# Optimization experiments

Measured on AMD Instinct MI355X. Metric: run time of the kernel, lower is better.

## Reference

```python
import jax, jax.numpy as jnp
import numpy as np

# dims (see shape_source): emb_dim=256, input_size=256 -> d_model=1024
B, L = 8, 1024
QUES = 4000
EMB = 256
DM = 1024          # input_size + 768
DI = 2048          # expand * d_model
N = 16             # d_state
DTR = 64           # dt_rank = ceil(d_model/16)
K = 4              # d_conv
EPS = 1e-12


def setup_inputs() -> dict:
    key = jax.random.key(0)
    ks = jax.random.split(key, 16)
    s = 0.02
    nrm = lambda k, sh: jax.random.normal(k, sh, dtype=jnp.float32) * s
    return {
        "x": jax.random.randint(ks[0], (B, L), 0, 2 * QUES + 1),
        "q_id": jax.random.randint(ks[1], (B, L), 0, QUES),
        "emb_table": nrm(ks[2], (2 * QUES + 1, EMB)),
        "ques_cont": nrm(ks[3], (QUES, 768)),
        "ln0_g": jnp.ones((DM,), jnp.float32),
        "ln0_b": jnp.zeros((DM,), jnp.float32),
        "in_proj_w": nrm(ks[4], (2 * DI, DM)),
        "conv_w": nrm(ks[5], (DI, K)),
        "conv_b": jnp.zeros((DI,), jnp.float32),
        "x_proj_w": nrm(ks[6], (DTR + 2 * N, DI)),
        "dt_proj_w": nrm(ks[7], (DI, DTR)),
        "dt_proj_b": nrm(ks[8], (DI,)),
        "A_log": jnp.log(jax.random.uniform(ks[9], (DI, N), jnp.float32, 1.0, 16.0)),
        "D_param": jnp.ones((DI,), jnp.float32),
        "out_proj_w": nrm(ks[10], (DM, DI)),
        "ln1_g": jnp.ones((DM,), jnp.float32),
        "ln1_b": jnp.zeros((DM,), jnp.float32),
        "fc_w": nrm(ks[11], (QUES, DM)),
        "fc_b": jnp.zeros((QUES,), jnp.float32),
    }


def _ln(x, g, b):
    m = x.mean(-1, keepdims=True)
    v = ((x - m) ** 2).mean(-1, keepdims=True)
    return (x - m) / jnp.sqrt(v + EPS) * g + b


def _mamba(xm, in_proj_w, conv_w, conv_b, x_proj_w, dt_proj_w, dt_proj_b,
           A_log, D_param, out_proj_w):
    # xm: [B, L, DM]
    u_r = xm @ in_proj_w.T                           # [B, L, 2*DI]
    u, r = jnp.split(u_r, 2, axis=-1)                # each [B, L, DI]
    Lq = u.shape[1]
    # causal depthwise conv1d (padding=K-1, truncated to L)
    u_pad = jnp.pad(u, ((0, 0), (K - 1, 0), (0, 0)))
    conv = sum(u_pad[:, k:k + Lq, :] * conv_w[:, k] for k in range(K)) + conv_b
    u = jax.nn.silu(conv)
    dbl = u @ x_proj_w.T                             # [B, L, DTR+2N]
    dt, Bm, Cm = dbl[..., :DTR], dbl[..., DTR:DTR + N], dbl[..., DTR + N:]
    delta = jax.nn.softplus(dt @ dt_proj_w.T + dt_proj_b)   # [B, L, DI]
    A = -jnp.exp(A_log)                              # [DI, N]

    def step(h, ins):
        d_t, b_t, c_t, u_t = ins                     # [B,DI],[B,N],[B,N],[B,DI]
        dA = jnp.exp(d_t[:, :, None] * A)            # [B, DI, N]
        h = dA * h + d_t[:, :, None] * b_t[:, None, :] * u_t[:, :, None]
        y_t = jnp.einsum('bdn,bn->bd', h, c_t)
        return h, y_t

    xs = (delta.transpose(1, 0, 2), Bm.transpose(1, 0, 2),
          Cm.transpose(1, 0, 2), u.transpose(1, 0, 2))
    h0 = jnp.zeros((u.shape[0], DI, N), u.dtype)
    _, ys = jax.lax.scan(step, h0, xs)               # ys: [L, B, DI]
    y = ys.transpose(1, 0, 2) + u * D_param
    y = y * jax.nn.silu(r)
    return y @ out_proj_w.T                          # [B, L, DM]


def reference(x, q_id, emb_table, ques_cont, ln0_g, ln0_b, in_proj_w, conv_w,
              conv_b, x_proj_w, dt_proj_w, dt_proj_b, A_log, D_param,
              out_proj_w, ln1_g, ln1_b, fc_w, fc_b):
    x_e = emb_table[x]                               # [B, L, 256]
    x_c = ques_cont[q_id]                            # [B, L, 768]
    item = _ln(jnp.concatenate([x_e, x_c], axis=-1), ln0_g, ln0_b)
    # source loop applies every layer to item_emb; only the last layer's
    # output is used, so compute exactly that one layer (num_layers=2 branch).
    h = _mamba(item, in_proj_w, conv_w, conv_b, x_proj_w, dt_proj_w,
               dt_proj_b, A_log, D_param, out_proj_w)
    out = _ln(h + item, ln1_g, ln1_b)
    return jax.nn.sigmoid(out @ fc_w.T + fc_b)       # [B, L, QUES]
```

## Files before the change

### kernel.cpp

```cpp
#include <hip/hip_runtime.h>
#include <cstdint>
#include <cstddef>

#define L_SEQ 1024
#define BATCH 8
#define DMODEL 1024
#define DINNER 2048
#define NSTATE 16
#define DTRANK 64
#define NQ 4000
#define NROWS (BATCH * L_SEQ)
#define CH 32
#define NCH (L_SEQ / CH)

typedef float f32x4 __attribute__((ext_vector_type(4)));
typedef __bf16 bf16x8 __attribute__((ext_vector_type(8)));

#define AS1 __attribute__((address_space(1)))
#define AS3 __attribute__((address_space(3)))

#define VMCNT(n) asm volatile("s_waitcnt vmcnt(" #n ")" ::: "memory")
#define SBARRIER() asm volatile("s_barrier" ::: "memory")

__device__ __forceinline__ unsigned short f2bf(float f) {
  union { float f; unsigned int u; } c; c.f = f;
  unsigned int u = c.u;
  unsigned int r = u + 0x7fffu + ((u >> 16) & 1u);
  return (unsigned short)(r >> 16);
}

__device__ __forceinline__ float sigmoidf_(float x) { return 1.f / (1.f + expf(-x)); }

__global__ void cast_bf16_k(const float* __restrict__ src, unsigned short* __restrict__ dst, int n) {
  int i = blockIdx.x * blockDim.x + threadIdx.x;
  if (i < n) dst[i] = f2bf(src[i]);
}

__device__ __forceinline__ float blk_sum(float v, float* s) {
  #pragma unroll
  for (int o = 32; o > 0; o >>= 1) v += __shfl_down(v, o, 64);
  int w = threadIdx.x >> 6;
  if ((threadIdx.x & 63) == 0) s[w] = v;
  __syncthreads();
  float r = s[0] + s[1] + s[2] + s[3];
  __syncthreads();
  return r;
}

__global__ __launch_bounds__(256) void embed_ln0_k(
    const int* __restrict__ x, const int* __restrict__ qid,
    const float* __restrict__ emb, const float* __restrict__ qc,
    const float* __restrict__ g, const float* __restrict__ bta,
    float* __restrict__ item, unsigned short* __restrict__ item_bf)
{
  __shared__ float sbuf[4];
  int i = blockIdx.x;
  int t = threadIdx.x;
  float4 v;
  if (t < 64) v = *(const float4*)&emb[(size_t)x[i] * 256 + t * 4];
  else        v = *(const float4*)&qc[(size_t)qid[i] * 768 + t * 4 - 256];
  float tot = blk_sum(v.x + v.y + v.z + v.w, sbuf);
  float mean = tot * (1.f / 1024.f);
  float dx = v.x - mean, dy = v.y - mean, dz = v.z - mean, dw = v.w - mean;
  float var = blk_sum(dx*dx + dy*dy + dz*dz + dw*dw, sbuf) * (1.f / 1024.f);
  float rstd = rsqrtf(var + 1e-12f);
  float vals[4] = {dx, dy, dz, dw};
  size_t rb = (size_t)i * 1024;
  #pragma unroll
  for (int j = 0; j < 4; j++) {
    int c = t * 4 + j;
    float o = vals[j] * rstd * g[c] + bta[c];
    item[rb + c] = o;
    item_bf[rb + c] = f2bf(o);
  }
}

template <int EPI>
__global__ __launch_bounds__(256) void gemm_bt_k(
    const unsigned short* __restrict__ A, const unsigned short* __restrict__ Bw,
    float* __restrict__ C, const float* __restrict__ bias,
    unsigned short* __restrict__ aux,
    int M, int N, int K)
{
  __shared__ __align__(16) unsigned short As[128 * 64];
  __shared__ __align__(16) unsigned short Bs[128 * 64];
  const int tid = threadIdx.x;
  const int m0 = blockIdx.x * 128;
  const int n0 = blockIdx.y * 128;
  const int w = tid >> 6, lane = tid & 63;
  const int wrow = (w >> 1) * 64, wcol = (w & 1) * 64;
  const int quad = lane >> 4, lid = lane & 15;

  const int srow = lane >> 3;
  const int schunk = (lane & 7) ^ srow;

  const unsigned short* Abase = A + (size_t)(m0 + w * 8 + srow) * K + schunk * 8;
  const unsigned short* Bbase[4];
  #pragma unroll
  for (int i = 0; i < 4; i++) {
    int rB = n0 + w * 8 + i * 32 + srow;
    if (rB > N - 1) rB = N - 1;
    Bbase[i] = Bw + (size_t)rB * K + schunk * 8;
  }

  f32x4 acc[4][4] = {};

  for (int k0 = 0; k0 < K; k0 += 64) {
    #pragma unroll
    for (int i = 0; i < 4; i++) {
      int rA = w * 8 + i * 32;
      __builtin_amdgcn_global_load_lds(
          (const AS1 unsigned int*)(Abase + (size_t)i * 32 * K + k0),
          (AS3 unsigned int*)&As[rA * 64], 16, 0, 0);
      __builtin_amdgcn_global_load_lds(
          (const AS1 unsigned int*)(Bbase[i] + k0),
          (AS3 unsigned int*)&Bs[rA * 64], 16, 0, 0);
    }
    __syncthreads();
    #pragma unroll
    for (int kk = 0; kk < 64; kk += 32) {
      bf16x8 af[4], bfr[4];
      #pragma unroll
      for (int mi = 0; mi < 4; mi++) {
        int r = wrow + mi * 16 + lid;
        int slot = ((kk >> 3) + quad) ^ (lid & 7);
        af[mi] = *(const bf16x8*)&As[r * 64 + slot * 8];
      }
      #pragma unroll
      for (int ni = 0; ni < 4; ni++) {
        int r = wcol + ni * 16 + lid;
        int slot = ((kk >> 3) + quad) ^ (lid & 7);
        bfr[ni] = *(const bf16x8*)&Bs[r * 64 + slot * 8];
      }
      #pragma unroll
      for (int mi = 0; mi < 4; mi++)
        #pragma unroll
        for (int ni = 0; ni < 4; ni++)
          acc[mi][ni] = __builtin_amdgcn_mfma_f32_16x16x32_bf16(af[mi], bfr[ni], acc[mi][ni], 0, 0, 0);
    }
    __syncthreads();
  }

  #pragma unroll
  for (int mi = 0; mi < 4; mi++) {
    #pragma unroll
    for (int ni = 0; ni < 4; ni++) {
      int col = n0 + wcol + ni * 16 + lid;
      if (col >= N) continue;
      #pragma unroll
      for (int r = 0; r < 4; r++) {
        int row = m0 + wrow + mi * 16 + quad * 4 + r;
        float v = acc[mi][ni][r];
        if (EPI == 1) v = sigmoidf_(v + bias[col]);
        if (EPI == 2) { float xx = v + bias[col]; v = fmaxf(xx, 0.f) + log1pf(expf(-fabsf(xx))); }
        C[(size_t)row * N + col] = v;
        if (EPI == 3 && col < 64) aux[(size_t)row * 64 + col] = f2bf(v);
      }
    }
  }
}

template <int BN, int EPI>
__global__ __launch_bounds__(512, 2) void gemm_pipe_k(
    const unsigned short* __restrict__ A, const unsigned short* __restrict__ Bw,
    float* __restrict__ C, const float* __restrict__ bias,
    int M, int N, int K)
{
  constexpr int NB = BN / 64;
  constexpr int BJ = (BN == 256) ? 2 : 1;
  constexpr int NI = 2 + BJ;

  __shared__ __align__(16) unsigned short As[3][256 * 32];
  __shared__ __align__(16) unsigned short Bs[3][BN * 32];

  const int tid = threadIdx.x;
  const int gx = gridDim.x;
  const int nwg = gx * gridDim.y;
  int bid = blockIdx.y * gx + blockIdx.x;
  bid = (bid & 7) * (nwg >> 3) + (bid >> 3);
  const int m0 = (bid % gx) * 256;
  const int n0 = (bid / gx) * BN;

  const int w = tid >> 6, lane = tid & 63;
  const int wm = w >> 2, wn = w & 3;
  const int quad = lane >> 4, lid = lane & 15;

  const int srow = lane >> 2;
  const int sch  = ((lane & 3) ^ ((lane >> 3) & 3)) * 8;

  const unsigned short* Ag[2];
  int AsegE[2];
  #pragma unroll
  for (int j = 0; j < 2; j++) {
    Ag[j] = A + (size_t)(m0 + 32 * w + 16 * j + srow) * K + sch;
    AsegE[j] = (w * 2 + j) * 512;
  }
  const unsigned short* Bg[BJ];
  int BsegE[BJ];
  #pragma unroll
  for (int j = 0; j < BJ; j++) {
    int rB = n0 + (BN == 256 ? 32 * w + 16 * j : 16 * w) + srow;
    if (rB > N - 1) rB = N - 1;
    Bg[j] = Bw + (size_t)rB * K + sch;
    BsegE[j] = (BN == 256 ? (w * 2 + j) : w) * 512;
  }

  auto stage = [&](int buf, int t) {
    const int ko = t * 32;
    #pragma unroll
    for (int j = 0; j < 2; j++)
      __builtin_amdgcn_global_load_lds(
          (const AS1 unsigned int*)(Ag[j] + ko),
          (AS3 unsigned int*)&As[buf][AsegE[j]], 16, 0, 0);
    #pragma unroll
    for (int j = 0; j < BJ; j++)
      __builtin_amdgcn_global_load_lds(
          (const AS1 unsigned int*)(Bg[j] + ko),
          (AS3 unsigned int*)&Bs[buf][BsegE[j]], 16, 0, 0);
  };

  const int slot8 = (quad ^ ((lid >> 1) & 3)) * 8;
  const int aoff = (wm * 128 + lid) * 32 + slot8;
  const int boff = (wn * (BN / 4) + lid) * 32 + slot8;

  f32x4 acc[8][NB] = {};
  const int nt = K >> 5;

  stage(0, 0);
  stage(1, 1);
  if constexpr (NI == 4) VMCNT(4); else VMCNT(3);
  SBARRIER();

  int bR = 0, bS = 2;
  for (int t = 0; t < nt; ++t) {
    const bool more = (t + 2 < nt);
    if (more) stage(bS, t + 2);
    __builtin_amdgcn_sched_barrier(0);

    bf16x8 af[8], bfr[NB];
    #pragma unroll
    for (int ni = 0; ni < NB; ni++) bfr[ni] = *(const bf16x8*)&Bs[bR][boff + ni * 512];
    #pragma unroll
    for (int mi = 0; mi < 8; mi++)  af[mi]  = *(const bf16x8*)&As[bR][aoff + mi * 512];

    __builtin_amdgcn_s_setprio(1);
    #pragma unroll
    for (int mi = 0; mi < 8; mi++)
      #pragma unroll
      for (int ni = 0; ni < NB; ni++)
        acc[mi][ni] = __builtin_amdgcn_mfma_f32_16x16x32_bf16(af[mi], bfr[ni], acc[mi][ni], 0, 0, 0);
    __builtin_amdgcn_s_setprio(0);

    __builtin_amdgcn_sched_barrier(0);
    if (more) { if constexpr (NI == 4) VMCNT(4); else VMCNT(3); }
    else VMCNT(0);
    SBARRIER();
    bR = (bR + 1 == 3) ? 0 : bR + 1;
    bS = (bS + 1 == 3) ? 0 : bS + 1;
  }

  #pragma unroll
  for (int mi = 0; mi < 8; mi++) {
    #pragma unroll
    for (int ni = 0; ni < NB; ni++) {
      int col = n0 + wn * (BN / 4) + ni * 16 + lid;
      if (col >= N) continue;
      #pragma unroll
      for (int r = 0; r < 4; r++) {
        int row = m0 + wm * 128 + mi * 16 + quad * 4 + r;
        float v = acc[mi][ni][r];
        if (EPI == 1) v = sigmoidf_(v + bias[col]);
        C[(size_t)row * N + col] = v;
      }
    }
  }
}

__global__ void conv_silu_k(const float* __restrict__ u_r, const float* __restrict__ w,
                            const float* __restrict__ cb, float* __restrict__ uc,
                            unsigned short* __restrict__ uc_bf)
{
  int idx = blockIdx.x * blockDim.x + threadIdx.x;
  if (idx >= BATCH * L_SEQ * DINNER) return;
  int d = idx & (DINNER - 1);
  int l = (idx >> 11) & (L_SEQ - 1);
  int b = idx >> 21;
  float4 wv = ((const float4*)w)[d];
  size_t rb = ((size_t)b * L_SEQ + l) * (2 * DINNER) + d;
  float acc = cb[d];
  acc += wv.w * u_r[rb];
  if (l >= 1) acc += wv.z * u_r[rb - (2 * DINNER)];
  if (l >= 2) acc += wv.y * u_r[rb - 2 * (2 * DINNER)];
  if (l >= 3) acc += wv.x * u_r[rb - 3 * (2 * DINNER)];
  float s = acc * sigmoidf_(acc);
  uc[idx] = s;
  uc_bf[idx] = f2bf(s);
}

__global__ void a2_k(const float* __restrict__ Alog, float* __restrict__ a2t)
{
  int i = blockIdx.x * blockDim.x + threadIdx.x;
  if (i >= DINNER * NSTATE) return;
  int d = i >> 4, n = i & 15;
  a2t[n * DINNER + d] = -expf(Alog[i]) * 1.4426950408889634f;
}

__global__ __launch_bounds__(64) void scan1_k(
    const float* __restrict__ dlt, const float* __restrict__ uc,
    const float* __restrict__ dbl, const float* __restrict__ a2t,
    float* __restrict__ Pbuf, float* __restrict__ Qbuf)
{
  int c = blockIdx.x;
  int dg = blockIdx.y;
  int b = blockIdx.z;
  int d = dg * 64 + threadIdx.x;
  float a2[NSTATE], P[NSTATE], q[NSTATE];
  #pragma unroll
  for (int n = 0; n < NSTATE; n++) {
    a2[n] = a2t[n * DINNER + d];
    P[n] = 1.f; q[n] = 0.f;
  }
  size_t base = ((size_t)(b * L_SEQ + c * CH)) * DINNER + d;
  const float* bc = dbl + (size_t)(b * L_SEQ + c * CH) * 96 + 64;
  for (int t = 0; t < CH; t++) {
    float dl = dlt[base];
    float du = dl * uc[base];
    #pragma unroll
    for (int n = 0; n < NSTATE; n++) {
      float dA = exp2f(dl * a2[n]);
      q[n] = dA * q[n] + du * bc[n];
      P[n] *= dA;
    }
    base += DINNER;
    bc += 96;
  }
  size_t ob = ((size_t)((b * NCH + c) * NSTATE)) * DINNER + d;
  #pragma unroll
  for (int n = 0; n < NSTATE; n++) {
    Pbuf[ob + (size_t)n * DINNER] = P[n];
    Qbuf[ob + (size_t)n * DINNER] = q[n];
  }
}

__global__ void scan_carry_k(const float* __restrict__ Pbuf, float* __restrict__ Qbuf)
{
  int idx = blockIdx.x * blockDim.x + threadIdx.x;
  if (idx >= BATCH * NSTATE * DINNER) return;
  int d = idx & (DINNER - 1);
  int n = (idx >> 11) & 15;
  int b = idx >> 15;
  float h = 0.f;
  for (int c = 0; c < NCH; c++) {
    size_t o = ((size_t)((b * NCH + c) * NSTATE + n)) * DINNER + d;
    float P = Pbuf[o];
    float q = Qbuf[o];
    Qbuf[o] = h;
    h = P * h + q;
  }
}

__global__ __launch_bounds__(64) void scan2_k(
    const float* __restrict__ dlt, const float* __restrict__ uc,
    const float* __restrict__ dbl, const float* __restrict__ a2t,
    const float* __restrict__ Qbuf, const float* __restrict__ u_r,
    const float* __restrict__ Dp, unsigned short* __restrict__ ybf)
{
  int c = blockIdx.x;
  int dg = blockIdx.y;
  int b = blockIdx.z;
  int d = dg * 64 + threadIdx.x;
  float a2[NSTATE], h[NSTATE];
  size_t ob = ((size_t)((b * NCH + c) * NSTATE)) * DINNER + d;
  #pragma unroll
  for (int n = 0; n < NSTATE; n++) {
    a2[n] = a2t[n * DINNER + d];
    h[n] = Qbuf[ob + (size_t)n * DINNER];
  }
  float Dd = Dp[d];
  size_t base = ((size_t)(b * L_SEQ + c * CH)) * DINNER + d;
  const float* bc = dbl + (size_t)(b * L_SEQ + c * CH) * 96 + 64;
  const float* rp = u_r + (size_t)(b * L_SEQ + c * CH) * (2 * DINNER) + DINNER + d;
  for (int t = 0; t < CH; t++) {
    float dl = dlt[base];
    float uval = uc[base];
    float du = dl * uval;
    float yv = 0.f;
    #pragma unroll
    for (int n = 0; n < NSTATE; n++) {
      float dA = exp2f(dl * a2[n]);
      h[n] = dA * h[n] + du * bc[n];
      yv += h[n] * bc[NSTATE + n];
    }
    float rv = *rp;
    float val = (yv + uval * Dd) * (rv * sigmoidf_(rv));
    ybf[base] = f2bf(val);
    base += DINNER;
    bc += 96;
    rp += 2 * DINNER;
  }
}

__global__ __launch_bounds__(256) void ln1_k(
    const float* __restrict__ mamba, const float* __restrict__ item,
    const float* __restrict__ g, const float* __restrict__ bta,
    unsigned short* __restrict__ out_bf)
{
  __shared__ float sbuf[4];
  int i = blockIdx.x;
  int t = threadIdx.x;
  size_t rb = (size_t)i * 1024 + t * 4;
  float4 v = *(const float4*)&mamba[rb];
  float4 w4 = *(const float4*)&item[rb];
  v.x += w4.x; v.y += w4.y; v.z += w4.z; v.w += w4.w;
  float tot = blk_sum(v.x + v.y + v.z + v.w, sbuf);
  float mean = tot * (1.f / 1024.f);
  float dx = v.x - mean, dy = v.y - mean, dz = v.z - mean, dw = v.w - mean;
  float var = blk_sum(dx*dx + dy*dy + dz*dz + dw*dw, sbuf) * (1.f / 1024.f);
  float rstd = rsqrtf(var + 1e-12f);
  float vals[4] = {dx, dy, dz, dw};
  #pragma unroll
  for (int j = 0; j < 4; j++) {
    int c = t * 4 + j;
    out_bf[(size_t)i * 1024 + c] = f2bf(vals[j] * rstd * g[c] + bta[c]);
  }
}

extern "C" void kernel_launch(void* const* d_in, const int* in_sizes, int n_in,
                              void* d_out, int out_size, void* d_ws, size_t ws_size,
                              hipStream_t stream)
{
  (void)in_sizes; (void)n_in; (void)out_size; (void)ws_size;
  const int*   x     = (const int*)d_in[0];
  const int*   qid   = (const int*)d_in[1];
  const float* emb   = (const float*)d_in[2];
  const float* qc    = (const float*)d_in[3];
  const float* ln0g  = (const float*)d_in[4];
  const float* ln0b  = (const float*)d_in[5];
  const float* w_in  = (const float*)d_in[6];
  const float* convw = (const float*)d_in[7];
  const float* convb = (const float*)d_in[8];
  const float* w_x   = (const float*)d_in[9];
  const float* w_dt  = (const float*)d_in[10];
  const float* dtb   = (const float*)d_in[11];
  const float* Alog  = (const float*)d_in[12];
  const float* Dp    = (const float*)d_in[13];
  const float* w_out = (const float*)d_in[14];
  const float* ln1g  = (const float*)d_in[15];
  const float* ln1b  = (const float*)d_in[16];
  const float* w_fc  = (const float*)d_in[17];
  const float* fcb   = (const float*)d_in[18];
  float* out = (float*)d_out;

  char* base = (char*)d_ws;
  size_t off = 0;
  auto carve = [&](size_t bytes) -> char* {
    char* p = base + off;
    off = (off + bytes + 255) & ~(size_t)255;
    return p;
  };
  float* item  = (float*)carve((size_t)NROWS * 1024 * 4);
  float* u_r   = (float*)carve((size_t)NROWS * 4096 * 4);
  float* uc    = (float*)carve((size_t)NROWS * 2048 * 4);
  float* dbl   = (float*)carve((size_t)NROWS * 96 * 4);
  float* dlt   = (float*)carve((size_t)NROWS * 2048 * 4);
  float* mamba = (float*)carve((size_t)NROWS * 1024 * 4);
  unsigned short* bfbuf  = (unsigned short*)carve((size_t)NROWS * 2048 * 2);
  unsigned short* bw_in  = (unsigned short*)carve((size_t)4096 * 1024 * 2);
  unsigned short* bw_x   = (unsigned short*)carve((size_t)96 * 2048 * 2);
  unsigned short* bw_dt  = (unsigned short*)carve((size_t)2048 * 64 * 2);
  unsigned short* bw_out = (unsigned short*)carve((size_t)1024 * 2048 * 2);
  unsigned short* bw_fc  = (unsigned short*)carve((size_t)4000 * 1024 * 2);
  float* a2t   = (float*)carve((size_t)DINNER * NSTATE * 4);

  unsigned short* dt_bf = (unsigned short*)mamba;
  float* Pbuf = mamba;
  float* Qbuf = (float*)bfbuf;
  unsigned short* y_bf = (unsigned short*)mamba;
  float* mamba_out = u_r;

  auto cv = [&](const float* s, unsigned short* dst, int n) {
    cast_bf16_k<<<(n + 255) / 256, 256, 0, stream>>>(s, dst, n);
  };
  cv(w_in,  bw_in,  4096 * 1024);
  cv(w_x,   bw_x,   96 * 2048);
  cv(w_dt,  bw_dt,  2048 * 64);
  cv(w_out, bw_out, 1024 * 2048);
  cv(w_fc,  bw_fc,  4000 * 1024);
  a2_k<<<(DINNER * NSTATE + 255) / 256, 256, 0, stream>>>(Alog, a2t);

  embed_ln0_k<<<NROWS, 256, 0, stream>>>(x, qid, emb, qc, ln0g, ln0b, item, bfbuf);

  gemm_pipe_k<256, 0><<<dim3(32, 16), 512, 0, stream>>>(bfbuf, bw_in, u_r, nullptr, NROWS, 4096, 1024);

  conv_silu_k<<<(NROWS * DINNER) / 256, 256, 0, stream>>>(u_r, convw, convb, uc, bfbuf);

  gemm_bt_k<3><<<dim3(64, 1), 256, 0, stream>>>(bfbuf, bw_x, dbl, nullptr, dt_bf, NROWS, 96, 2048);

  gemm_bt_k<2><<<dim3(64, 16), 256, 0, stream>>>(dt_bf, bw_dt, dlt, dtb, nullptr, NROWS, 2048, 64);

  scan1_k<<<dim3(NCH, 32, BATCH), 64, 0, stream>>>(dlt, uc, dbl, a2t, Pbuf, Qbuf);
  scan_carry_k<<<(BATCH * NSTATE * DINNER) / 256, 256, 0, stream>>>(Pbuf, Qbuf);
  scan2_k<<<dim3(NCH, 32, BATCH), 64, 0, stream>>>(dlt, uc, dbl, a2t, Qbuf, u_r, Dp, y_bf);

  gemm_pipe_k<128, 0><<<dim3(32, 8), 512, 0, stream>>>(y_bf, bw_out, mamba_out, nullptr, NROWS, 1024, 2048);

  ln1_k<<<NROWS, 256, 0, stream>>>(mamba_out, item, ln1g, ln1b, bfbuf);

  gemm_pipe_k<256, 1><<<dim3(32, 16), 512, 0, stream>>>(bfbuf, bw_fc, out, fcb, NROWS, 4000, 1024);
}
```

Baseline: 923.9 us.

## Restructure bf16 GEMM pipeline into 4-slice, 8-phase staging with split MFMA groups

Replaces the 3-buffer, one-K-tile-per-iteration GEMM loop with a 4-slice LDS layout that covers two K=32 tiles per iteration. The iteration is split into four phases. Each phase issues a separate A or B load unit and runs half of the MFMA block, with barriers between phases. The goal is finer interleaving of global-to-LDS loads with MFMA work and deeper prefetch, to hide memory latency in the three large GEMMs. The cost is more barriers per K step and more LDS per block, which could reduce occupancy.

Result: slower. 1.094 ms (+18.4%).

```diff
diff --git a/kernel.cpp b/kernel.cpp
--- a/kernel.cpp
+++ b/kernel.cpp
@@ -20,6 +20,7 @@
 #define AS3 __attribute__((address_space(3)))
 
 #define VMCNT(n) asm volatile("s_waitcnt vmcnt(" #n ")" ::: "memory")
+#define LGKMCNT0() asm volatile("s_waitcnt lgkmcnt(0)" ::: "memory")
 #define SBARRIER() asm volatile("s_barrier" ::: "memory")
 
 __device__ __forceinline__ unsigned short f2bf(float f) {
@@ -161,17 +162,18 @@
 }
 
 template <int BN, int EPI>
-__global__ __launch_bounds__(512, 2) void gemm_pipe_k(
+__global__ __launch_bounds__(512, 2) void gemm8p_k(
     const unsigned short* __restrict__ A, const unsigned short* __restrict__ Bw,
     float* __restrict__ C, const float* __restrict__ bias,
     int M, int N, int K)
 {
   constexpr int NB = BN / 64;
-  constexpr int BJ = (BN == 256) ? 2 : 1;
-  constexpr int NI = 2 + BJ;
-
-  __shared__ __align__(16) unsigned short As[3][256 * 32];
-  __shared__ __align__(16) unsigned short Bs[3][BN * 32];
+  constexpr int BJ = BN / 128;
+  constexpr int ASLICE = 256 * 32;
+  constexpr int BSLICE = BN * 32;
+
+  __shared__ __align__(16) unsigned short As[4 * ASLICE];
+  __shared__ __align__(16) unsigned short Bs[4 * BSLICE];
 
   const int tid = threadIdx.x;
   const int gx = gridDim.x;
@@ -185,38 +187,43 @@
   const int wm = w >> 2, wn = w & 3;
   const int quad = lane >> 4, lid = lane & 15;
 
-  const int srow = lane >> 2;
-  const int sch  = ((lane & 3) ^ ((lane >> 3) & 3)) * 8;
-
+  const int g8 = ((lane & 3) ^ ((lane >> 3) & 3)) * 8;
   const unsigned short* Ag[2];
   int AsegE[2];
   #pragma unroll
   for (int j = 0; j < 2; j++) {
-    Ag[j] = A + (size_t)(m0 + 32 * w + 16 * j + srow) * K + sch;
+    Ag[j] = A + (size_t)(m0 + w * 32 + j * 16 + (lane >> 2)) * K + g8;
     AsegE[j] = (w * 2 + j) * 512;
   }
   const unsigned short* Bg[BJ];
   int BsegE[BJ];
   #pragma unroll
   for (int j = 0; j < BJ; j++) {
-    int rB = n0 + (BN == 256 ? 32 * w + 16 * j : 16 * w) + srow;
+    int rB = n0 + (w * BJ + j) * 16 + (lane >> 2);
     if (rB > N - 1) rB = N - 1;
-    Bg[j] = Bw + (size_t)rB * K + sch;
-    BsegE[j] = (BN == 256 ? (w * 2 + j) : w) * 512;
-  }
-
-  auto stage = [&](int buf, int t) {
-    const int ko = t * 32;
-    #pragma unroll
-    for (int j = 0; j < 2; j++)
-      __builtin_amdgcn_global_load_lds(
-          (const AS1 unsigned int*)(Ag[j] + ko),
-          (AS3 unsigned int*)&As[buf][AsegE[j]], 16, 0, 0);
-    #pragma unroll
-    for (int j = 0; j < BJ; j++)
-      __builtin_amdgcn_global_load_lds(
-          (const AS1 unsigned int*)(Bg[j] + ko),
-          (AS3 unsigned int*)&Bs[buf][BsegE[j]], 16, 0, 0);
+    Bg[j] = Bw + (size_t)rB * K + g8;
+    BsegE[j] = (w * BJ + j) * 512;
+  }
+
+  const int NT = K >> 6;
+  auto stage_unit = [&](int u) {
+    if (u >= 4 * NT) return;
+    const int tu = u >> 2, ty = u & 3;
+    const int sl = (tu & 1) * 2 + (ty >> 1);
+    const size_t kofs = (size_t)(tu << 6) + ((ty >> 1) << 5);
+    if ((ty & 1) == 0) {
+      #pragma unroll
+      for (int j = 0; j < 2; j++)
+        __builtin_amdgcn_global_load_lds(
+            (const AS1 unsigned int*)(Ag[j] + kofs),
+            (AS3 unsigned int*)&As[sl * ASLICE + AsegE[j]], 16, 0, 0);
+    } else {
+      #pragma unroll
+      for (int j = 0; j < BJ; j++)
+        __builtin_amdgcn_global_load_lds(
+            (const AS1 unsigned int*)(Bg[j] + kofs),
+            (AS3 unsigned int*)&Bs[sl * BSLICE + BsegE[j]], 16, 0, 0);
+    }
   };
 
   const int slot8 = (quad ^ ((lid >> 1) & 3)) * 8;
@@ -224,39 +231,78 @@
   const int boff = (wn * (BN / 4) + lid) * 32 + slot8;
 
   f32x4 acc[8][NB] = {};
-  const int nt = K >> 5;
-
-  stage(0, 0);
-  stage(1, 1);
-  if constexpr (NI == 4) VMCNT(4); else VMCNT(3);
+
+  #pragma unroll
+  for (int u = 0; u < 7; u++) stage_unit(u);
+  if constexpr (BJ == 2) VMCNT(6); else VMCNT(5);
   SBARRIER();
 
-  int bR = 0, bS = 2;
-  for (int t = 0; t < nt; ++t) {
-    const bool more = (t + 2 < nt);
-    if (more) stage(bS, t + 2);
+  for (int T = 0; T < NT; ++T) {
+    const int ab = (T & 1) * 2;
+    const unsigned short* Asl0 = &As[(ab + 0) * ASLICE];
+    const unsigned short* Asl1 = &As[(ab + 1) * ASLICE];
+    const unsigned short* Bsl0 = &Bs[(ab + 0) * BSLICE];
+    const unsigned short* Bsl1 = &Bs[(ab + 1) * BSLICE];
+
+    bf16x8 af[8], bfr[NB];
+
+    stage_unit(4 * T + 7);
     __builtin_amdgcn_sched_barrier(0);
-
-    bf16x8 af[8], bfr[NB];
-    #pragma unroll
-    for (int ni = 0; ni < NB; ni++) bfr[ni] = *(const bf16x8*)&Bs[bR][boff + ni * 512];
-    #pragma unroll
-    for (int mi = 0; mi < 8; mi++)  af[mi]  = *(const bf16x8*)&As[bR][aoff + mi * 512];
-
+    #pragma unroll
+    for (int ni = 0; ni < NB; ni++) bfr[ni] = *(const bf16x8*)&Bsl0[boff + ni * 512];
+    #pragma unroll
+    for (int mi = 0; mi < 8; mi++)  af[mi]  = *(const bf16x8*)&Asl0[aoff + mi * 512];
     __builtin_amdgcn_s_setprio(1);
     #pragma unroll
-    for (int mi = 0; mi < 8; mi++)
+    for (int mi = 0; mi < 4; mi++)
       #pragma unroll
       for (int ni = 0; ni < NB; ni++)
         acc[mi][ni] = __builtin_amdgcn_mfma_f32_16x16x32_bf16(af[mi], bfr[ni], acc[mi][ni], 0, 0, 0);
     __builtin_amdgcn_s_setprio(0);
-
+    LGKMCNT0();
     __builtin_amdgcn_sched_barrier(0);
-    if (more) { if constexpr (NI == 4) VMCNT(4); else VMCNT(3); }
-    else VMCNT(0);
     SBARRIER();
-    bR = (bR + 1 == 3) ? 0 : bR + 1;
-    bS = (bS + 1 == 3) ? 0 : bS + 1;
+
+    stage_unit(4 * T + 8);
+    __builtin_amdgcn_sched_barrier(0);
+    __builtin_amdgcn_s_setprio(1);
+    #pragma unroll
+    for (int mi = 4; mi < 8; mi++)
+      #pragma unroll
+      for (int ni = 0; ni < NB; ni++)
+        acc[mi][ni] = __builtin_amdgcn_mfma_f32_16x16x32_bf16(af[mi], bfr[ni], acc[mi][ni], 0, 0, 0);
+    __builtin_amdgcn_s_setprio(0);
+    SBARRIER();
+
+    stage_unit(4 * T + 9);
+    __builtin_amdgcn_sched_barrier(0);
+    #pragma unroll
+    for (int ni = 0; ni < NB; ni++) bfr[ni] = *(const bf16x8*)&Bsl1[boff + ni * 512];
+    #pragma unroll
+    for (int mi = 0; mi < 8; mi++)  af[mi]  = *(const bf16x8*)&Asl1[aoff + mi * 512];
+    __builtin_amdgcn_s_setprio(1);
+    #pragma unroll
+    for (int mi = 0; mi < 4; mi++)
+      #pragma unroll
+      for (int ni = 0; ni < NB; ni++)
+        acc[mi][ni] = __builtin_amdgcn_mfma_f32_16x16x32_bf16(af[mi], bfr[ni], acc[mi][ni], 0, 0, 0);
+    __builtin_amdgcn_s_setprio(0);
+    LGKMCNT0();
+    __builtin_amdgcn_sched_barrier(0);
+    SBARRIER();
+
+    stage_unit(4 * T + 10);
+    __builtin_amdgcn_sched_barrier(0);
+    __builtin_amdgcn_s_setprio(1);
+    #pragma unroll
+    for (int mi = 4; mi < 8; mi++)
+      #pragma unroll
+      for (int ni = 0; ni < NB; ni++)
+        acc[mi][ni] = __builtin_amdgcn_mfma_f32_16x16x32_bf16(af[mi], bfr[ni], acc[mi][ni], 0, 0, 0);
+    __builtin_amdgcn_s_setprio(0);
+    if (T >= NT - 2) { VMCNT(0); }
+    else { if constexpr (BJ == 2) VMCNT(6); else VMCNT(5); }
+    SBARRIER();
   }
 
   #pragma unroll
@@ -490,7 +536,7 @@
 
   embed_ln0_k<<<NROWS, 256, 0, stream>>>(x, qid, emb, qc, ln0g, ln0b, item, bfbuf);
 
-  gemm_pipe_k<256, 0><<<dim3(32, 16), 512, 0, stream>>>(bfbuf, bw_in, u_r, nullptr, NROWS, 4096, 1024);
+  gemm8p_k<256, 0><<<dim3(32, 16), 512, 0, stream>>>(bfbuf, bw_in, u_r, nullptr, NROWS, 4096, 1024);
 
   conv_silu_k<<<(NROWS * DINNER) / 256, 256, 0, stream>>>(u_r, convw, convb, uc, bfbuf);
 
@@ -502,9 +548,9 @@
   scan_carry_k<<<(BATCH * NSTATE * DINNER) / 256, 256, 0, stream>>>(Pbuf, Qbuf);
   scan2_k<<<dim3(NCH, 32, BATCH), 64, 0, stream>>>(dlt, uc, dbl, a2t, Qbuf, u_r, Dp, y_bf);
 
-  gemm_pipe_k<128, 0><<<dim3(32, 8), 512, 0, stream>>>(y_bf, bw_out, mamba_out, nullptr, NROWS, 1024, 2048);
+  gemm8p_k<128, 0><<<dim3(32, 8), 512, 0, stream>>>(y_bf, bw_out, mamba_out, nullptr, NROWS, 1024, 2048);
 
   ln1_k<<<NROWS, 256, 0, stream>>>(mamba_out, item, ln1g, ln1b, bfbuf);
 
-  gemm_pipe_k<256, 1><<<dim3(32, 16), 512, 0, stream>>>(bfbuf, bw_fc, out, fcb, NROWS, 4000, 1024);
-}
+  gemm8p_k<256, 1><<<dim3(32, 16), 512, 0, stream>>>(bfbuf, bw_fc, out, fcb, NROWS, 4000, 1024);
+}
```
